# Performance work log

Hardware: AMD Instinct MI355X
Metric: run time of the kernel (lower is better)

## Reference

```python
import jax, jax.numpy as jnp
import numpy as np

B, T, U, H, M, K, C = 64, 800, 80, 512, 20, 10, 80  # batch, tsteps, char len, rnn_size, nmixtures, kmixtures, char_vec_len


def _lstm(x, W, Uw, b):
    """Keras-semantics LSTM (gate order i,f,g,o), zero initial state. x: [B,T,D] -> [B,T,H]."""
    xg = jnp.einsum('btd,dh->bth', x, W) + b  # precompute input contribution
    h0 = jnp.zeros((x.shape[0], Uw.shape[0]), x.dtype)
    c0 = jnp.zeros_like(h0)

    def step(carry, zt):
        h, c = carry
        z = zt + h @ Uw
        i, f, g, o = jnp.split(z, 4, axis=-1)
        c = jax.nn.sigmoid(f) * c + jax.nn.sigmoid(i) * jnp.tanh(g)
        h = jax.nn.sigmoid(o) * jnp.tanh(c)
        return (h, c), h

    _, hs = jax.lax.scan(step, (h0, c0), jnp.swapaxes(xg, 0, 1))
    return jnp.swapaxes(hs, 0, 1)


def _forward(stroke_data, char_seq, kappa0, W0, U0, b0, W1, U1, b1, W2, U2, b2, Wa, ba, Wm, bm):
    lstm0_out = _lstm(stroke_data, W0, U0, b0)  # [B,T,H]
    # Attention window: the per-timestep loop in the source only carries kappa,
    # which is a running sum of exp(kappa_offset) -> vectorize via cumsum.
    abk = jnp.exp(jnp.einsum('bth,hk->btk', lstm0_out, Wa) + ba)  # [B,T,3K]
    alpha, beta, koff = jnpp_split = jnp.split(abk, 3, axis=-1)
    kappa = kappa0[:, None, :, 0] + jnp.cumsum(koff, axis=1)  # [B,T,K]
    u = jnp.arange(char_seq.shape[1], dtype=stroke_data.dtype)  # [U]
    # phi: [B,T,U] = sum_k alpha * exp(-beta * (kappa - u)^2)
    phi = jnp.sum(alpha[..., None] * jnp.exp(-beta[..., None] * (kappa[..., None] - u) ** 2), axis=2)
    windows = jnp.einsum('btu,buc->btc', phi, char_seq)  # [B,T,C]
    aug = jnp.concatenate([lstm0_out, windows, stroke_data], axis=-1)
    lstm1_out = _lstm(aug, W1, U1, b1)
    lstm2_out = _lstm(lstm1_out, W2, U2, b2)
    mdn = jnp.einsum('bth,hn->btn', lstm2_out, Wm) + bm  # [B,T,1+6M]
    eos_hat = mdn[..., 0:1]
    pi_hat, mu1, mu2, s1_hat, s2_hat, rho_hat = jnp.split(mdn[..., 1:], 6, axis=-1)
    return jnp.concatenate([
        jax.nn.sigmoid(-eos_hat),
        jax.nn.softmax(pi_hat, axis=-1),
        mu1, mu2,
        jnp.exp(s1_hat), jnp.exp(s2_hat),
        jnp.tanh(rho_hat),
    ], axis=-1)  # [B,T,1+6M]


def setup_inputs() -> dict:
    key = jax.random.key(0)
    ks = jax.random.split(key, 12)
    init = lambda k, shape: jax.random.truncated_normal(k, -2.0, 2.0, shape, jnp.float32) * 0.075
    return {
        'stroke_data': jax.random.normal(ks[0], (B, T, 3), jnp.float32),
        'char_seq': jax.nn.one_hot(jax.random.randint(ks[1], (B, U), 0, C), C, dtype=jnp.float32),
        'kappa0': jnp.zeros((B, K, 1), jnp.float32),
        'W0': init(ks[2], (3, 4 * H)), 'U0': init(ks[3], (H, 4 * H)), 'b0': jnp.zeros((4 * H,)),
        'W1': init(ks[4], (H + C + 3, 4 * H)), 'U1': init(ks[5], (H, 4 * H)), 'b1': jnp.zeros((4 * H,)),
        'W2': init(ks[6], (H, 4 * H)), 'U2': init(ks[7], (H, 4 * H)), 'b2': jnp.zeros((4 * H,)),
        'Wa': init(ks[8], (H, 3 * K)),
        'ba': -3.0 + 0.25 * jax.random.truncated_normal(ks[9], -2.0, 2.0, (3 * K,), jnp.float32),
        'Wm': init(ks[10], (H, 1 + 6 * M)), 'bm': jnp.zeros((1 + 6 * M,)),
    }


def reference(stroke_data, char_seq, kappa0, W0, U0, b0, W1, U1, b1, W2, U2, b2, Wa, ba, Wm, bm):
    return _forward(stroke_data, char_seq, kappa0, W0, U0, b0, W1, U1, b1, W2, U2, b2, Wa, ba, Wm, bm)
```

## Files before the change

kernel.cpp:

```cpp
#include <hip/hip_runtime.h>

typedef unsigned short u16;
typedef unsigned int u32;
typedef short v8s __attribute__((ext_vector_type(8)));
typedef float v4f __attribute__((ext_vector_type(4)));
typedef unsigned int v4u __attribute__((ext_vector_type(4)));
typedef unsigned int v2u __attribute__((ext_vector_type(2)));

#define MFMA16 __builtin_amdgcn_mfma_f32_16x16x32_bf16

constexpr int TT = 800;
constexpr int NBLK = 178;

constexpr int AUGB  = 2240;
constexpr int AUG2B = 2048;

constexpr size_t AUGR_OFF  = 131072;
constexpr size_t AUG2R_OFF = AUGR_OFF + (size_t)4 * 64 * AUGB;
constexpr size_t WAT_OFF   = AUG2R_OFF + (size_t)4 * 64 * AUG2B;
constexpr size_t WS_ZERO   = WAT_OFF + (size_t)32 * 512 * 2;

constexpr u32 SMEM_BYTES = 82944;

enum { G_S0D = 0, G_SAD = 1, G_S1D = 2, G_S2D = 3, G_S1R = 4, G_SAR = 5, G_S2R = 6, G_SMR = 7 };

__device__ __forceinline__ float bf2f(u16 u) { return __uint_as_float(((u32)u) << 16); }
__device__ __forceinline__ u16 f2bf(float f) {
    u32 x = __float_as_uint(f);
    return (u16)((x + 0x7fffu + ((x >> 16) & 1u)) >> 16);
}
__device__ __forceinline__ short f2bfs(float f) { return (short)f2bf(f); }
__device__ __forceinline__ float sigf(float x) { return 1.f / (1.f + __expf(-x)); }
__device__ __forceinline__ float tanhf2(float x) { return 1.f - 2.f / (1.f + __expf(2.f * x)); }

__device__ __forceinline__ __amdgpu_buffer_rsrc_t mkrsrc(const void* p) {
    return __builtin_amdgcn_make_buffer_rsrc((void*)p, (short)0, -1, 0x00020000);
}
__device__ __forceinline__ v4u ldu4(__amdgpu_buffer_rsrc_t r, int off) {
    return __builtin_amdgcn_raw_buffer_load_b128(r, off, 0, 17);
}
__device__ __forceinline__ v2u ldu8(__amdgpu_buffer_rsrc_t r, int off) {
    return __builtin_amdgcn_raw_buffer_load_b64(r, off, 0, 17);
}
__device__ __forceinline__ void stq8(__amdgpu_buffer_rsrc_t r, int off, u16 a, u16 b, u16 c, u16 d) {
    v2u t; t[0] = (u32)a | ((u32)b << 16); t[1] = (u32)c | ((u32)d << 16);
    __builtin_amdgcn_raw_buffer_store_b64(t, r, off, 0, 17);
}
__device__ __forceinline__ void stq4(__amdgpu_buffer_rsrc_t r, int off, u16 a, u16 b) {
    u32 t = (u32)a | ((u32)b << 16);
    __builtin_amdgcn_raw_buffer_store_b32(t, r, off, 0, 17);
}

__device__ __forceinline__ void publish(u32* ctrl, int g, int t, int sub) {
    __hip_atomic_fetch_add(ctrl + g * 4096 + (t & 3) * 1024 + (sub & 15) * 64, 1u,
                           __ATOMIC_RELAXED, __HIP_MEMORY_SCOPE_AGENT);
}
__device__ __forceinline__ void wait4(u32* ctrl,
    int g0, int t0, u32 n0, int m0, int g1, int t1, u32 n1, int m1,
    int g2, int t2, u32 n2, int m2, int g3, int t3, u32 n3, int m3)
{
    if (threadIdx.x < 64) {
        const int lane = threadIdx.x;
        const int cl = lane >> 4, k = lane & 15;
        int g, tt, mb; u32 nn;
        if (cl == 0)      { g = g0; tt = t0; nn = n0; mb = m0; }
        else if (cl == 1) { g = g1; tt = t1; nn = n1; mb = m1; }
        else if (cl == 2) { g = g2; tt = t2; nn = n2; mb = m2; }
        else              { g = g3; tt = t3; nn = n3; mb = m3; }
        const u32 tgt = (g >= 0 && tt >= 0) ? nn * (u32)((tt >> 2) + 1) : 0u;
        u32* p = (tgt > 0) ? (ctrl + g * 4096 + (tt & 3) * 1024 + (mb + (k & 7)) * 64) : (u32*)0;
        int sp = 0;
        for (;;) {
            u32 v = p ? __hip_atomic_load(p, __ATOMIC_RELAXED, __HIP_MEMORY_SCOPE_AGENT) : 0u;
            v += __shfl_xor(v, 1); v += __shfl_xor(v, 2);
            v += __shfl_xor(v, 4); v += __shfl_xor(v, 8);
            const bool bad = (tgt > 0) && (v < tgt);
            if (__ballot(bad) == 0ull) break;
            if (sp >= 2) __builtin_amdgcn_s_sleep(4);
            else if (sp == 1) __builtin_amdgcn_s_sleep(1);
            sp++;
        }
    }
    __syncthreads();
}

__global__ void wat_init(const float* __restrict__ Wa, u16* __restrict__ WaT) {
    __amdgpu_buffer_rsrc_t r = mkrsrc(WaT);
    for (int idx = blockIdx.x * 256 + threadIdx.x; idx < 32 * 512 / 2; idx += gridDim.x * 256) {
        const int e0 = idx * 2, e1 = e0 + 1;
        const int n0 = e0 >> 9, k0 = e0 & 511;
        const int n1 = e1 >> 9, k1 = e1 & 511;
        const u16 a = (n0 < 30) ? f2bf(Wa[k0 * 30 + n0]) : (u16)0;
        const u16 b = (n1 < 30) ? f2bf(Wa[k1 * 30 + n1]) : (u16)0;
        stq4(r, idx * 4, a, b);
    }
}

__global__ __launch_bounds__(256, 1) void hw_main(
    const float* __restrict__ stroke, const float* __restrict__ charseq, const float* __restrict__ kappa0,
    const float* __restrict__ W0, const float* __restrict__ U0, const float* __restrict__ b0,
    const float* __restrict__ W1, const float* __restrict__ U1, const float* __restrict__ b1,
    const float* __restrict__ W2, const float* __restrict__ U2, const float* __restrict__ b2,
    const float* __restrict__ ba, const float* __restrict__ Wm, const float* __restrict__ bm,
    float* __restrict__ out, char* __restrict__ ws)
{
    extern __shared__ __align__(16) char smem[];
    u32* ctrl = (u32*)ws;
    u16* augr  = (u16*)(ws + AUGR_OFF);
    u16* aug2r = (u16*)(ws + AUG2R_OFF);
    const u16* WaT = (const u16*)(ws + WAT_OFF);

    const int blk = blockIdx.x, tid = threadIdx.x;
    const int wave = tid >> 6, lane = tid & 63;
    const int quad = lane >> 4, l15 = lane & 15;

    if (blk < 32) {
        const int cs = blk & 15, mg = blk >> 4;
        const int mb = mg * 8, sub = mb + (cs & 7);
        __amdgpu_buffer_rsrc_t ra = mkrsrc(augr);
        u16*   aL  = (u16*)smem;
        float* zb  = (float*)(smem + 33280);
        float* w0s = (float*)(smem + 50176);
        float* b0s = (float*)(smem + 51712);
        if (tid < 128) {
            const int cn2 = (tid >> 5) * 512 + cs * 32 + (tid & 31);
            b0s[tid] = b0[cn2];
            #pragma unroll
            for (int d = 0; d < 3; d++) w0s[d * 128 + tid] = W0[d * 2048 + cn2];
        }
        v8s bw0[16], bw1[16];
        {
            const int cnA = wave * 512 + cs * 32 + l15;
            const int cnB = cnA + 16;
            #pragma unroll
            for (int kc = 0; kc < 16; kc++)
                #pragma unroll
                for (int j = 0; j < 8; j++) {
                    const int k = kc * 32 + quad * 8 + j;
                    bw0[kc][j] = f2bfs(U0[k * 2048 + cnA]);
                    bw1[kc][j] = f2bfs(U0[k * 2048 + cnB]);
                }
        }
        float cst[4] = {0.f, 0.f, 0.f, 0.f};
        const int bl_ = tid & 31;
        const int bpre = mg * 32 + bl_;
        __syncthreads();
        #pragma unroll 1
        for (int t = 0; t < TT; t++) {
            const float xx0 = stroke[(bpre * TT + t) * 3 + 0];
            const float xx1 = stroke[(bpre * TT + t) * 3 + 1];
            const float xx2 = stroke[(bpre * TT + t) * 3 + 2];
            wait4(ctrl, G_S0D, t - 1, 32, mb, G_S1R, t - 4, 64, mb, G_SAR, t - 4, 16, mb, -1, 0, 0, 0);
            {
                const int base = (((t + 3) & 3) * 64 + mg * 32) * AUGB;
                #pragma unroll
                for (int c8 = 0; c8 < 8; c8++) {
                    const int c = tid + 256 * c8;
                    const int row = c >> 6, off = c & 63;
                    v4u d = ldu4(ra, base + row * AUGB + off * 16);
                    *(v4u*)((char*)aL + row * 1040 + off * 16) = d;
                }
            }
            __syncthreads();
            v4f c0a = {0,0,0,0}, c0b = {0,0,0,0}, c1a = {0,0,0,0}, c1b = {0,0,0,0};
            const int xo = quad * 16;
            #pragma unroll
            for (int kc = 0; kc < 16; kc++) {
                v8s x0 = *(const v8s*)((const char*)aL + l15 * 1040 + kc * 64 + xo);
                v8s x1 = *(const v8s*)((const char*)aL + (16 + l15) * 1040 + kc * 64 + xo);
                c0a = MFMA16(x0, bw0[kc], c0a, 0, 0, 0);
                c1a = MFMA16(x0, bw1[kc], c1a, 0, 0, 0);
                c0b = MFMA16(x1, bw0[kc], c0b, 0, 0, 0);
                c1b = MFMA16(x1, bw1[kc], c1b, 0, 0, 0);
            }
            const int n0 = wave * 32 + l15, n1 = n0 + 16;
            #pragma unroll
            for (int r = 0; r < 4; r++) {
                zb[(quad * 4 + r) * 132 + n0] = c0a[r];
                zb[(quad * 4 + r) * 132 + n1] = c1a[r];
                zb[(16 + quad * 4 + r) * 132 + n0] = c0b[r];
                zb[(16 + quad * 4 + r) * 132 + n1] = c1b[r];
            }
            __syncthreads();
            {
                const int bl = tid & 31, jj = tid >> 5;
                const int b = mg * 32 + bl;
                u16 hv[4];
                #pragma unroll
                for (int m = 0; m < 4; m++) {
                    const int j = jj * 4 + m;
                    float z[4];
                    #pragma unroll
                    for (int g = 0; g < 4; g++) {
                        const int n = g * 32 + j;
                        z[g] = zb[bl * 132 + n] + b0s[n] + xx0 * w0s[n] + xx1 * w0s[128 + n] + xx2 * w0s[256 + n];
                    }
                    const float cc = sigf(z[1]) * cst[m] + sigf(z[0]) * tanhf2(z[2]);
                    cst[m] = cc;
                    hv[m] = f2bf(sigf(z[3]) * tanhf2(cc));
                }
                stq8(ra, ((t & 3) * 64 + b) * AUGB + (cs * 32 + jj * 4) * 2, hv[0], hv[1], hv[2], hv[3]);
            }
            __syncthreads();
            if (tid == 0) publish(ctrl, G_S0D, t, sub);
        }
    } else if (blk < 96) {
        const int q = blk - 32, cs = q >> 1, mg = q & 1;
        const int mb = mg * 8, sub = mb + (cs & 7);
        __amdgpu_buffer_rsrc_t ra = mkrsrc(augr);
        __amdgpu_buffer_rsrc_t r2 = mkrsrc(aug2r);
        u16*   aL  = (u16*)smem;
        float* zb  = (float*)(smem + 72192);
        float* b1s = (float*)(smem + 80896);
        if (tid < 64) b1s[tid] = b1[(tid >> 4) * 512 + cs * 16 + (tid & 15)];
        v8s bw[35];
        {
            const int cn = wave * 512 + cs * 16 + l15;
            #pragma unroll
            for (int kc = 0; kc < 35; kc++)
                #pragma unroll
                for (int j = 0; j < 8; j++) {
                    const int k = kc * 32 + quad * 8 + j;
                    short v = 0;
                    if (k < 595) v = f2bfs(W1[k * 2048 + cn]);
                    else if (k >= 596 && k < 1108) v = f2bfs(U1[(k - 596) * 2048 + cn]);
                    bw[kc][j] = v;
                }
        }
        if (tid < 32) { v4u z4 = {0,0,0,0}; *(v4u*)((char*)aL + tid * 2256 + 2224) = z4; }
        float cst[2] = {0.f, 0.f};
        __syncthreads();
        #pragma unroll 1
        for (int t = 0; t < TT; t++) {
            wait4(ctrl, G_S0D, t, 32, mb, G_SAD, t, 16, mb, G_S2R, t - 4, 64, mb, -1, 0, 0, 0);
            {
                const int base = ((t & 3) * 64 + mg * 32) * AUGB;
                #pragma unroll
                for (int c10 = 0; c10 < 10; c10++) {
                    const int c = tid + 256 * c10;
                    if (c < 2400) {
                        const int row = c / 75, off = c - row * 75;
                        v4u d = ldu4(ra, base + row * AUGB + off * 16);
                        *(v4u*)((char*)aL + row * 2256 + off * 16) = d;
                    }
                }
            }
            __syncthreads();
            if (tid == 0) publish(ctrl, G_S1R, t, sub);
            wait4(ctrl, G_S1D, t - 1, 64, mb, -1, 0, 0, 0, -1, 0, 0, 0, -1, 0, 0, 0);
            {
                const int base = ((t & 3) * 64 + mg * 32) * AUGB;
                if (tid < 32) {
                    v2u d8 = ldu8(ra, base + tid * AUGB + 1192);
                    *(v2u*)((char*)aL + tid * 2256 + 1192) = d8;
                }
                #pragma unroll
                for (int c8 = 0; c8 < 8; c8++) {
                    const int c = tid + 256 * c8;
                    const int row = c >> 6, off = 75 + (c & 63);
                    v4u d = ldu4(ra, base + row * AUGB + off * 16);
                    *(v4u*)((char*)aL + row * 2256 + off * 16) = d;
                }
            }
            v4f c0 = {0,0,0,0}, c1 = {0,0,0,0};
            const int xo = quad * 16;
            #pragma unroll
            for (int kc = 0; kc < 18; kc++) {
                v8s x0 = *(const v8s*)((const char*)aL + l15 * 2256 + kc * 64 + xo);
                v8s x1 = *(const v8s*)((const char*)aL + (16 + l15) * 2256 + kc * 64 + xo);
                c0 = MFMA16(x0, bw[kc], c0, 0, 0, 0);
                c1 = MFMA16(x1, bw[kc], c1, 0, 0, 0);
            }
            __syncthreads();
            #pragma unroll
            for (int kc = 18; kc < 35; kc++) {
                v8s x0 = *(const v8s*)((const char*)aL + l15 * 2256 + kc * 64 + xo);
                v8s x1 = *(const v8s*)((const char*)aL + (16 + l15) * 2256 + kc * 64 + xo);
                c0 = MFMA16(x0, bw[kc], c0, 0, 0, 0);
                c1 = MFMA16(x1, bw[kc], c1, 0, 0, 0);
            }
            #pragma unroll
            for (int r = 0; r < 4; r++) {
                zb[(quad * 4 + r) * 68 + wave * 17 + l15] = c0[r];
                zb[(16 + quad * 4 + r) * 68 + wave * 17 + l15] = c1[r];
            }
            __syncthreads();
            {
                const int bl = tid & 31, jj = tid >> 5;
                const int b = mg * 32 + bl;
                u16 hv[2];
                #pragma unroll
                for (int m = 0; m < 2; m++) {
                    const int j = jj * 2 + m;
                    float z[4];
                    #pragma unroll
                    for (int g = 0; g < 4; g++)
                        z[g] = zb[bl * 68 + g * 17 + j] + b1s[g * 16 + j];
                    const float cc = sigf(z[1]) * cst[m] + sigf(z[0]) * tanhf2(z[2]);
                    cst[m] = cc;
                    hv[m] = f2bf(sigf(z[3]) * tanhf2(cc));
                }
                stq4(ra, (((t + 1) & 3) * 64 + b) * AUGB + (596 + cs * 16 + jj * 2) * 2, hv[0], hv[1]);
                stq4(r2, ((t & 3) * 64 + b) * AUG2B + (cs * 16 + jj * 2) * 2, hv[0], hv[1]);
            }
            __syncthreads();
            if (tid == 0) publish(ctrl, G_S1D, t, sub);
        }
    } else if (blk < 160) {
        const int q = blk - 96, cs = q >> 1, mg = q & 1;
        const int mb = mg * 8, sub = mb + (cs & 7);
        __amdgpu_buffer_rsrc_t r2 = mkrsrc(aug2r);
        u16*   aL  = (u16*)smem;
        float* zb  = (float*)(smem + 66048);
        float* b2s = (float*)(smem + 74752);
        if (tid < 64) b2s[tid] = b2[(tid >> 4) * 512 + cs * 16 + (tid & 15)];
        v8s bw[32];
        {
            const int cn = wave * 512 + cs * 16 + l15;
            #pragma unroll
            for (int kc = 0; kc < 32; kc++)
                #pragma unroll
                for (int j = 0; j < 8; j++) {
                    const int k = kc * 32 + quad * 8 + j;
                    bw[kc][j] = (k < 512) ? f2bfs(W2[k * 2048 + cn]) : f2bfs(U2[(k - 512) * 2048 + cn]);
                }
        }
        float cst[2] = {0.f, 0.f};
        __syncthreads();
        #pragma unroll 1
        for (int t = 0; t < TT; t++) {
            wait4(ctrl, G_S1D, t, 64, mb, G_SMR, t - 4, 2, mb, -1, 0, 0, 0, -1, 0, 0, 0);
            {
                const int base = ((t & 3) * 64 + mg * 32) * AUG2B;
                #pragma unroll
                for (int c8 = 0; c8 < 8; c8++) {
                    const int c = tid + 256 * c8;
                    const int row = c >> 6, off = c & 63;
                    v4u d = ldu4(r2, base + row * AUG2B + off * 16);
                    *(v4u*)((char*)aL + row * 2064 + off * 16) = d;
                }
            }
            __syncthreads();
            if (tid == 0) publish(ctrl, G_S2R, t, sub);
            wait4(ctrl, G_S2D, t - 1, 64, mb, -1, 0, 0, 0, -1, 0, 0, 0, -1, 0, 0, 0);
            {
                const int base = ((t & 3) * 64 + mg * 32) * AUG2B;
                #pragma unroll
                for (int c8 = 0; c8 < 8; c8++) {
                    const int c = tid + 256 * c8;
                    const int row = c >> 6, off = 64 + (c & 63);
                    v4u d = ldu4(r2, base + row * AUG2B + off * 16);
                    *(v4u*)((char*)aL + row * 2064 + off * 16) = d;
                }
            }
            v4f c0 = {0,0,0,0}, c1 = {0,0,0,0};
            const int xo = quad * 16;
            #pragma unroll
            for (int kc = 0; kc < 16; kc++) {
                v8s x0 = *(const v8s*)((const char*)aL + l15 * 2064 + kc * 64 + xo);
                v8s x1 = *(const v8s*)((const char*)aL + (16 + l15) * 2064 + kc * 64 + xo);
                c0 = MFMA16(x0, bw[kc], c0, 0, 0, 0);
                c1 = MFMA16(x1, bw[kc], c1, 0, 0, 0);
            }
            __syncthreads();
            #pragma unroll
            for (int kc = 16; kc < 32; kc++) {
                v8s x0 = *(const v8s*)((const char*)aL + l15 * 2064 + kc * 64 + xo);
                v8s x1 = *(const v8s*)((const char*)aL + (16 + l15) * 2064 + kc * 64 + xo);
                c0 = MFMA16(x0, bw[kc], c0, 0, 0, 0);
                c1 = MFMA16(x1, bw[kc], c1, 0, 0, 0);
            }
            #pragma unroll
            for (int r = 0; r < 4; r++) {
                zb[(quad * 4 + r) * 68 + wave * 17 + l15] = c0[r];
                zb[(16 + quad * 4 + r) * 68 + wave * 17 + l15] = c1[r];
            }
            __syncthreads();
            {
                const int bl = tid & 31, jj = tid >> 5;
                const int b = mg * 32 + bl;
                u16 hv[2];
                #pragma unroll
                for (int m = 0; m < 2; m++) {
                    const int j = jj * 2 + m;
                    float z[4];
                    #pragma unroll
                    for (int g = 0; g < 4; g++)
                        z[g] = zb[bl * 68 + g * 17 + j] + b2s[g * 16 + j];
                    const float cc = sigf(z[1]) * cst[m] + sigf(z[0]) * tanhf2(z[2]);
                    cst[m] = cc;
                    hv[m] = f2bf(sigf(z[3]) * tanhf2(cc));
                }
                stq4(r2, (((t + 1) & 3) * 64 + b) * AUG2B + (512 + cs * 16 + jj * 2) * 2, hv[0], hv[1]);
            }
            __syncthreads();
            if (tid == 0) publish(ctrl, G_S2D, t, sub);
        }
    } else if (blk < 176) {
        const int a = blk - 160;
        const int mg = a >> 3, mb = mg * 8, sub = mb + (a & 7);
        const int b = a * 4 + wave;
        __amdgpu_buffer_rsrc_t ra = mkrsrc(augr);
        u16*   watl = (u16*)smem;
        u16*   hrow = (u16*)(smem + 33280);
        float* phis = (float*)(smem + 37440);
        u16*   idxs = (u16*)(smem + 38720);
        {
            #pragma unroll
            for (int c8 = 0; c8 < 8; c8++) {
                const int c = tid + 256 * c8;
                const int row = c >> 6, off = c & 63;
                *(v4u*)((char*)watl + row * 1040 + off * 16) = *(const v4u*)(WaT + row * 512 + off * 8);
            }
        }
        #pragma unroll
        for (int rep = 0; rep < 2; rep++) {
            const int u = rep * 64 + lane;
            if (u < 80) {
                int c = 0;
                #pragma unroll 1
                for (int cc = 0; cc < 80; cc++)
                    if (charseq[b * 6400 + u * 80 + cc] > 0.5f) c = cc;
                idxs[wave * 80 + u] = (u16)c;
            }
        }
        float kap = (lane < 10) ? kappa0[b * 10 + lane] : 0.f;
        const float baf = (lane < 30) ? ba[lane] : 0.f;
        const int nn = lane & 31;
        const int k0 = (lane >> 5) * 256;
        const u16* wrow = watl + nn * 520 + k0;
        __syncthreads();
        #pragma unroll 1
        for (int t = 0; t < TT; t++) {
            float sx0 = 0.f, sx1 = 0.f;
            if (lane == 40) { sx0 = stroke[(b * TT + t) * 3 + 0]; sx1 = stroke[(b * TT + t) * 3 + 1]; }
            else if (lane == 41) { sx0 = stroke[(b * TT + t) * 3 + 2]; }
            wait4(ctrl, G_S0D, t, 32, mb, G_S1R, t - 4, 64, mb, -1, 0, 0, 0, -1, 0, 0, 0);
            {
                const int row = tid >> 6, off = tid & 63;
                v4u d = ldu4(ra, ((t & 3) * 64 + a * 4 + row) * AUGB + off * 16);
                *(v4u*)((char*)hrow + row * 1040 + off * 16) = d;
            }
            __syncthreads();
            if (tid == 0) publish(ctrl, G_SAR, t, sub);
            float acc = 0.f;
            #pragma unroll
            for (int kk = 0; kk < 32; kk++) {
                v8s hv = *(const v8s*)((const char*)hrow + wave * 1040 + (k0 + kk * 8) * 2);
                v8s wv = *(const v8s*)(wrow + kk * 8);
                #pragma unroll
                for (int e = 0; e < 8; e++) acc += bf2f((u16)hv[e]) * bf2f((u16)wv[e]);
            }
            acc += __shfl_xor(acc, 32);
            const float abk = __expf(acc + baf);
            const float kofv = __shfl(abk, 20 + (lane < 10 ? lane : 0));
            if (lane < 10) kap += kofv;
            const float u1f = (float)lane;
            float p1 = 0.f, p2 = 0.f;
            #pragma unroll
            for (int kk = 0; kk < 10; kk++) {
                const float al = __shfl(abk, kk);
                const float be = __shfl(abk, 10 + kk);
                const float kp = __shfl(kap, kk);
                const float d1 = kp - u1f, d2 = kp - (u1f + 64.f);
                p1 += al * __expf(-be * d1 * d1);
                p2 += al * __expf(-be * d2 * d2);
            }
            phis[wave * 80 + lane] = p1;
            if (lane < 16) phis[wave * 80 + 64 + lane] = p2;
            __syncthreads();
            const int db = (((t & 3) * 64 + b) * AUGB) + 512 * 2;
            if (lane < 40) {
                const int c0 = 2 * lane;
                float w0 = 0.f, w1 = 0.f;
                #pragma unroll 1
                for (int u = 0; u < 80; u++) {
                    const float pv = phis[wave * 80 + u];
                    const int ix = (int)idxs[wave * 80 + u];
                    w0 += (ix == c0)     ? pv : 0.f;
                    w1 += (ix == c0 + 1) ? pv : 0.f;
                }
                stq4(ra, db + c0 * 2, f2bf(w0), f2bf(w1));
            } else if (lane == 40) {
                stq4(ra, db + 80 * 2, f2bf(sx0), f2bf(sx1));
            } else if (lane == 41) {
                stq4(ra, db + 82 * 2, f2bf(sx0), (u16)0);
            }
            __syncthreads();
            if (tid == 0) publish(ctrl, G_SAD, t, sub);
        }
    } else {
        const int mgs = blk - 176;
        const int mb = mgs * 8, sub = mb;
        __amdgpu_buffer_rsrc_t r2 = mkrsrc(aug2r);
        u16*   aL = (u16*)smem;
        float* zb = (float*)(smem + 33280);
        v8s bw0[16], bw1[16];
        {
            const int nA = wave * 32 + l15, nB = nA + 16;
            #pragma unroll
            for (int kc = 0; kc < 16; kc++)
                #pragma unroll
                for (int j = 0; j < 8; j++) {
                    const int k = kc * 32 + quad * 8 + j;
                    bw0[kc][j] = (nA < 121) ? f2bfs(Wm[k * 121 + nA]) : (short)0;
                    bw1[kc][j] = (nB < 121) ? f2bfs(Wm[k * 121 + nB]) : (short)0;
                }
        }
        __syncthreads();
        #pragma unroll 1
        for (int t = 0; t < TT; t++) {
            wait4(ctrl, G_S2D, t, 64, mb, -1, 0, 0, 0, -1, 0, 0, 0, -1, 0, 0, 0);
            {
                const int base = (((t + 1) & 3) * 64 + mgs * 32) * AUG2B + 1024;
                #pragma unroll
                for (int c8 = 0; c8 < 8; c8++) {
                    const int c = tid + 256 * c8;
                    const int row = c >> 6, off = c & 63;
                    v4u d = ldu4(r2, base + row * AUG2B + off * 16);
                    *(v4u*)((char*)aL + row * 1040 + off * 16) = d;
                }
            }
            __syncthreads();
            if (tid == 0) publish(ctrl, G_SMR, t, sub);
            v4f c0a = {0,0,0,0}, c0b = {0,0,0,0}, c1a = {0,0,0,0}, c1b = {0,0,0,0};
            const int xo = quad * 16;
            #pragma unroll
            for (int kc = 0; kc < 16; kc++) {
                v8s x0 = *(const v8s*)((const char*)aL + l15 * 1040 + kc * 64 + xo);
                v8s x1 = *(const v8s*)((const char*)aL + (16 + l15) * 1040 + kc * 64 + xo);
                c0a = MFMA16(x0, bw0[kc], c0a, 0, 0, 0);
                c1a = MFMA16(x0, bw1[kc], c1a, 0, 0, 0);
                c0b = MFMA16(x1, bw0[kc], c0b, 0, 0, 0);
                c1b = MFMA16(x1, bw1[kc], c1b, 0, 0, 0);
            }
            const int n0 = wave * 32 + l15, n1 = n0 + 16;
            #pragma unroll
            for (int r = 0; r < 4; r++) {
                zb[(quad * 4 + r) * 132 + n0] = c0a[r];
                zb[(quad * 4 + r) * 132 + n1] = c1a[r];
                zb[(16 + quad * 4 + r) * 132 + n0] = c0b[r];
                zb[(16 + quad * 4 + r) * 132 + n1] = c1b[r];
            }
            __syncthreads();
            {
                const int b8 = tid >> 3, g8 = tid & 7;
                const int b = mgs * 32 + b8;
                const float* zr = zb + b8 * 132;
                float* orow = out + ((size_t)(b * TT + t)) * 121;
                if (g8 == 0) {
                    orow[0] = sigf(-(zr[0] + bm[0]));
                    float mx = -1e30f;
                    float zv[20];
                    #pragma unroll 1
                    for (int nl = 1; nl <= 20; nl++) { zv[nl - 1] = zr[nl] + bm[nl]; mx = fmaxf(mx, zv[nl - 1]); }
                    float ss = 0.f;
                    #pragma unroll 1
                    for (int nl = 0; nl < 20; nl++) { zv[nl] = __expf(zv[nl] - mx); ss += zv[nl]; }
                    const float inv = 1.f / ss;
                    #pragma unroll 1
                    for (int nl = 0; nl < 20; nl++) orow[nl + 1] = zv[nl] * inv;
                } else if (g8 <= 2) {
                    const int s0 = 21 + (g8 - 1) * 20;
                    #pragma unroll 1
                    for (int nl = s0; nl < s0 + 20; nl++) orow[nl] = zr[nl] + bm[nl];
                } else if (g8 <= 4) {
                    const int s0 = 61 + (g8 - 3) * 20;
                    #pragma unroll 1
                    for (int nl = s0; nl < s0 + 20; nl++) orow[nl] = __expf(zr[nl] + bm[nl]);
                } else if (g8 <= 6) {
                    const int s0 = 101 + (g8 - 5) * 10;
                    #pragma unroll 1
                    for (int nl = s0; nl < s0 + 10; nl++) orow[nl] = tanhf2(zr[nl] + bm[nl]);
                }
            }
            __syncthreads();
        }
    }
}

extern "C" void kernel_launch(void* const* d_in, const int* in_sizes, int n_in,
                              void* d_out, int out_size, void* d_ws, size_t ws_size,
                              hipStream_t stream) {
    const float* stroke  = (const float*)d_in[0];
    const float* charseq = (const float*)d_in[1];
    const float* kappa0  = (const float*)d_in[2];
    const float* W0 = (const float*)d_in[3];
    const float* U0 = (const float*)d_in[4];
    const float* b0 = (const float*)d_in[5];
    const float* W1 = (const float*)d_in[6];
    const float* U1 = (const float*)d_in[7];
    const float* b1 = (const float*)d_in[8];
    const float* W2 = (const float*)d_in[9];
    const float* U2 = (const float*)d_in[10];
    const float* b2 = (const float*)d_in[11];
    const float* Wa = (const float*)d_in[12];
    const float* ba = (const float*)d_in[13];
    const float* Wm = (const float*)d_in[14];
    const float* bm = (const float*)d_in[15];
    char* ws = (char*)d_ws;

    static bool attr_done = false;
    if (!attr_done) {
        hipFuncSetAttribute((const void*)hw_main,
                            hipFuncAttributeMaxDynamicSharedMemorySize, SMEM_BYTES);
        attr_done = true;
    }

    hipMemsetAsync(d_ws, 0, WS_ZERO, stream);
    wat_init<<<8, 256, 0, stream>>>(Wa, (u16*)(ws + WAT_OFF));
    hw_main<<<NBLK, 256, SMEM_BYTES, stream>>>(stroke, charseq, kappa0, W0, U0, b0,
                                               W1, U1, b1, W2, U2, b2, ba, Wm, bm,
                                               (float*)d_out, ws);
}
```

Baseline: 8.748 ms.

## Split shared activation buffers into per-producer-block tiled layouts and use uncached polling

Replaces the row-major augmented activation buffers with separate per-layer buffers (h0, window, h1, h2), each laid out by producer column slice so every producer block writes one contiguous chunk and consumers gather tiles into LDS. The layer-1 K layout is realigned so the window/stroke segment is padded to a 32-wide chunk boundary. The window block now zero-fills the padding. Flag polling switches to an inline-asm buffer load with sc0/sc1 cache-bypass bits and a shorter sleep, aiming to cut cross-block sync latency and scattered small global writes. Risks include more complex gather indexing and more polling traffic.

```diff
diff --git a/kernel.cpp b/kernel.cpp
--- a/kernel.cpp
+++ b/kernel.cpp
@@ -12,15 +12,14 @@
 constexpr int TT = 800;
 constexpr int NBLK = 178;
 
-constexpr int AUGB  = 2240;
-constexpr int AUG2B = 2048;
-
-constexpr size_t AUGR_OFF  = 131072;
-constexpr size_t AUG2R_OFF = AUGR_OFF + (size_t)4 * 64 * AUGB;
-constexpr size_t WAT_OFF   = AUG2R_OFF + (size_t)4 * 64 * AUG2B;
-constexpr size_t WS_ZERO   = WAT_OFF + (size_t)32 * 512 * 2;
-
-constexpr u32 SMEM_BYTES = 82944;
+constexpr size_t H0_OFF  = 131072;
+constexpr size_t WIN_OFF = H0_OFF  + (size_t)4 * 2 * 16 * 2048;
+constexpr size_t H1_OFF  = WIN_OFF + (size_t)4 * 2 * 32 * 256;
+constexpr size_t H2_OFF  = H1_OFF  + (size_t)4 * 2 * 32 * 1024;
+constexpr size_t WAT_OFF = H2_OFF  + (size_t)4 * 2 * 32 * 1024;
+constexpr size_t WS_ZERO = WAT_OFF + (size_t)32 * 512 * 2;
+
+constexpr u32 SMEM_BYTES = 81920;
 
 enum { G_S0D = 0, G_SAD = 1, G_S1D = 2, G_S2D = 3, G_S1R = 4, G_SAR = 5, G_S2R = 6, G_SMR = 7 };
 
@@ -39,9 +38,6 @@
 __device__ __forceinline__ v4u ldu4(__amdgpu_buffer_rsrc_t r, int off) {
     return __builtin_amdgcn_raw_buffer_load_b128(r, off, 0, 17);
 }
-__device__ __forceinline__ v2u ldu8(__amdgpu_buffer_rsrc_t r, int off) {
-    return __builtin_amdgcn_raw_buffer_load_b64(r, off, 0, 17);
-}
 __device__ __forceinline__ void stq8(__amdgpu_buffer_rsrc_t r, int off, u16 a, u16 b, u16 c, u16 d) {
     v2u t; t[0] = (u32)a | ((u32)b << 16); t[1] = (u32)c | ((u32)d << 16);
     __builtin_amdgcn_raw_buffer_store_b64(t, r, off, 0, 17);
@@ -49,6 +45,22 @@
 __device__ __forceinline__ void stq4(__amdgpu_buffer_rsrc_t r, int off, u16 a, u16 b) {
     u32 t = (u32)a | ((u32)b << 16);
     __builtin_amdgcn_raw_buffer_store_b32(t, r, off, 0, 17);
+}
+
+__device__ __forceinline__ v4u mksrd(const void* p) {
+    v4u r;
+    r[0] = (u32)(size_t)p;
+    r[1] = (u32)((size_t)p >> 32);
+    r[2] = 0xFFFFFFFFu;
+    r[3] = 0x00020000u;
+    return r;
+}
+__device__ __forceinline__ u32 poll_ld(v4u srd, int off) {
+    u32 v;
+    asm volatile("buffer_load_dword %0, %1, %2, 0 offen sc0 sc1\n\t"
+                 "s_waitcnt vmcnt(0)"
+                 : "=v"(v) : "v"(off), "s"(srd) : "memory");
+    return v;
 }
 
 __device__ __forceinline__ void publish(u32* ctrl, int g, int t, int sub) {
@@ -68,15 +80,16 @@
         else if (cl == 2) { g = g2; tt = t2; nn = n2; mb = m2; }
         else              { g = g3; tt = t3; nn = n3; mb = m3; }
         const u32 tgt = (g >= 0 && tt >= 0) ? nn * (u32)((tt >> 2) + 1) : 0u;
-        u32* p = (tgt > 0) ? (ctrl + g * 4096 + (tt & 3) * 1024 + (mb + (k & 7)) * 64) : (u32*)0;
+        const v4u srd = mksrd(ctrl);
+        const int boff = (g >= 0) ? (g * 4096 + ((tt & 3)) * 1024 + (mb + (k & 7)) * 64) * 4 : 0;
         int sp = 0;
         for (;;) {
-            u32 v = p ? __hip_atomic_load(p, __ATOMIC_RELAXED, __HIP_MEMORY_SCOPE_AGENT) : 0u;
+            u32 v = (tgt > 0) ? poll_ld(srd, boff) : 0u;
             v += __shfl_xor(v, 1); v += __shfl_xor(v, 2);
             v += __shfl_xor(v, 4); v += __shfl_xor(v, 8);
             const bool bad = (tgt > 0) && (v < tgt);
             if (__ballot(bad) == 0ull) break;
-            if (sp >= 2) __builtin_amdgcn_s_sleep(4);
+            if (sp >= 2) __builtin_amdgcn_s_sleep(2);
             else if (sp == 1) __builtin_amdgcn_s_sleep(1);
             sp++;
         }
@@ -106,8 +119,10 @@
 {
     extern __shared__ __align__(16) char smem[];
     u32* ctrl = (u32*)ws;
-    u16* augr  = (u16*)(ws + AUGR_OFF);
-    u16* aug2r = (u16*)(ws + AUG2R_OFF);
+    u16* h0b  = (u16*)(ws + H0_OFF);
+    u16* winb = (u16*)(ws + WIN_OFF);
+    u16* h1b  = (u16*)(ws + H1_OFF);
+    u16* h2b  = (u16*)(ws + H2_OFF);
     const u16* WaT = (const u16*)(ws + WAT_OFF);
 
     const int blk = blockIdx.x, tid = threadIdx.x;
@@ -117,7 +132,7 @@
     if (blk < 32) {
         const int cs = blk & 15, mg = blk >> 4;
         const int mb = mg * 8, sub = mb + (cs & 7);
-        __amdgpu_buffer_rsrc_t ra = mkrsrc(augr);
+        __amdgpu_buffer_rsrc_t rh0 = mkrsrc(h0b);
         u16*   aL  = (u16*)smem;
         float* zb  = (float*)(smem + 33280);
         float* w0s = (float*)(smem + 50176);
@@ -142,8 +157,7 @@
                 }
         }
         float cst[4] = {0.f, 0.f, 0.f, 0.f};
-        const int bl_ = tid & 31;
-        const int bpre = mg * 32 + bl_;
+        const int bpre = mg * 32 + (tid & 31);
         __syncthreads();
         #pragma unroll 1
         for (int t = 0; t < TT; t++) {
@@ -152,13 +166,14 @@
             const float xx2 = stroke[(bpre * TT + t) * 3 + 2];
             wait4(ctrl, G_S0D, t - 1, 32, mb, G_S1R, t - 4, 64, mb, G_SAR, t - 4, 16, mb, -1, 0, 0, 0);
             {
-                const int base = (((t + 3) & 3) * 64 + mg * 32) * AUGB;
+                const int base = ((((t + 3) & 3) * 2 + mg) * 16) * 2048;
                 #pragma unroll
                 for (int c8 = 0; c8 < 8; c8++) {
                     const int c = tid + 256 * c8;
-                    const int row = c >> 6, off = c & 63;
-                    v4u d = ldu4(ra, base + row * AUGB + off * 16);
-                    *(v4u*)((char*)aL + row * 1040 + off * 16) = d;
+                    const int cs_ = c >> 7, w = c & 127;
+                    const int row = w >> 2, col16 = w & 3;
+                    v4u d = ldu4(rh0, base + cs_ * 2048 + w * 16);
+                    *(v4u*)((char*)aL + row * 1040 + cs_ * 64 + col16 * 16) = d;
                 }
             }
             __syncthreads();
@@ -184,7 +199,6 @@
             __syncthreads();
             {
                 const int bl = tid & 31, jj = tid >> 5;
-                const int b = mg * 32 + bl;
                 u16 hv[4];
                 #pragma unroll
                 for (int m = 0; m < 4; m++) {
@@ -199,7 +213,8 @@
                     cst[m] = cc;
                     hv[m] = f2bf(sigf(z[3]) * tanhf2(cc));
                 }
-                stq8(ra, ((t & 3) * 64 + b) * AUGB + (cs * 32 + jj * 4) * 2, hv[0], hv[1], hv[2], hv[3]);
+                const int off = (((t & 3) * 2 + mg) * 16 + cs) * 2048 + bl * 64 + jj * 8;
+                stq8(rh0, off, hv[0], hv[1], hv[2], hv[3]);
             }
             __syncthreads();
             if (tid == 0) publish(ctrl, G_S0D, t, sub);
@@ -207,8 +222,9 @@
     } else if (blk < 96) {
         const int q = blk - 32, cs = q >> 1, mg = q & 1;
         const int mb = mg * 8, sub = mb + (cs & 7);
-        __amdgpu_buffer_rsrc_t ra = mkrsrc(augr);
-        __amdgpu_buffer_rsrc_t r2 = mkrsrc(aug2r);
+        __amdgpu_buffer_rsrc_t rh0 = mkrsrc(h0b);
+        __amdgpu_buffer_rsrc_t rw  = mkrsrc(winb);
+        __amdgpu_buffer_rsrc_t rh1 = mkrsrc(h1b);
         u16*   aL  = (u16*)smem;
         float* zb  = (float*)(smem + 72192);
         float* b1s = (float*)(smem + 80896);
@@ -222,26 +238,34 @@
                 for (int j = 0; j < 8; j++) {
                     const int k = kc * 32 + quad * 8 + j;
                     short v = 0;
-                    if (k < 595) v = f2bfs(W1[k * 2048 + cn]);
-                    else if (k >= 596 && k < 1108) v = f2bfs(U1[(k - 596) * 2048 + cn]);
+                    if (kc < 19) { if (k < 595) v = f2bfs(W1[k * 2048 + cn]); }
+                    else v = f2bfs(U1[(k - 608) * 2048 + cn]);
                     bw[kc][j] = v;
                 }
         }
-        if (tid < 32) { v4u z4 = {0,0,0,0}; *(v4u*)((char*)aL + tid * 2256 + 2224) = z4; }
         float cst[2] = {0.f, 0.f};
         __syncthreads();
         #pragma unroll 1
         for (int t = 0; t < TT; t++) {
             wait4(ctrl, G_S0D, t, 32, mb, G_SAD, t, 16, mb, G_S2R, t - 4, 64, mb, -1, 0, 0, 0);
             {
-                const int base = ((t & 3) * 64 + mg * 32) * AUGB;
-                #pragma unroll
-                for (int c10 = 0; c10 < 10; c10++) {
-                    const int c = tid + 256 * c10;
-                    if (c < 2400) {
-                        const int row = c / 75, off = c - row * 75;
-                        v4u d = ldu4(ra, base + row * AUGB + off * 16);
-                        *(v4u*)((char*)aL + row * 2256 + off * 16) = d;
+                const int baseH = (((t & 3) * 2 + mg) * 16) * 2048;
+                const int baseW = (((t & 3) * 2 + mg) * 32) * 256;
+                #pragma unroll
+                for (int c8 = 0; c8 < 8; c8++) {
+                    const int c = tid + 256 * c8;
+                    const int cs_ = c >> 7, w = c & 127;
+                    const int row = w >> 2, col16 = w & 3;
+                    v4u d = ldu4(rh0, baseH + cs_ * 2048 + w * 16);
+                    *(v4u*)((char*)aL + row * 2256 + cs_ * 64 + col16 * 16) = d;
+                }
+                #pragma unroll
+                for (int c2 = 0; c2 < 2; c2++) {
+                    const int c = tid + 256 * c2;
+                    if (c < 384) {
+                        const int row = c / 12, off = c - row * 12;
+                        v4u d = ldu4(rw, baseW + row * 256 + off * 16);
+                        *(v4u*)((char*)aL + row * 2256 + 1024 + off * 16) = d;
                     }
                 }
             }
@@ -249,23 +273,20 @@
             if (tid == 0) publish(ctrl, G_S1R, t, sub);
             wait4(ctrl, G_S1D, t - 1, 64, mb, -1, 0, 0, 0, -1, 0, 0, 0, -1, 0, 0, 0);
             {
-                const int base = ((t & 3) * 64 + mg * 32) * AUGB;
-                if (tid < 32) {
-                    v2u d8 = ldu8(ra, base + tid * AUGB + 1192);
-                    *(v2u*)((char*)aL + tid * 2256 + 1192) = d8;
-                }
+                const int baseP = ((((t + 3) & 3) * 2 + mg) * 32) * 1024;
                 #pragma unroll
                 for (int c8 = 0; c8 < 8; c8++) {
                     const int c = tid + 256 * c8;
-                    const int row = c >> 6, off = 75 + (c & 63);
-                    v4u d = ldu4(ra, base + row * AUGB + off * 16);
-                    *(v4u*)((char*)aL + row * 2256 + off * 16) = d;
+                    const int cs_ = c >> 6, w = c & 63;
+                    const int row = w >> 1, col16 = w & 1;
+                    v4u d = ldu4(rh1, baseP + cs_ * 1024 + w * 16);
+                    *(v4u*)((char*)aL + row * 2256 + 1216 + cs_ * 32 + col16 * 16) = d;
                 }
             }
             v4f c0 = {0,0,0,0}, c1 = {0,0,0,0};
             const int xo = quad * 16;
             #pragma unroll
-            for (int kc = 0; kc < 18; kc++) {
+            for (int kc = 0; kc < 19; kc++) {
                 v8s x0 = *(const v8s*)((const char*)aL + l15 * 2256 + kc * 64 + xo);
                 v8s x1 = *(const v8s*)((const char*)aL + (16 + l15) * 2256 + kc * 64 + xo);
                 c0 = MFMA16(x0, bw[kc], c0, 0, 0, 0);
@@ -273,7 +294,7 @@
             }
             __syncthreads();
             #pragma unroll
-            for (int kc = 18; kc < 35; kc++) {
+            for (int kc = 19; kc < 35; kc++) {
                 v8s x0 = *(const v8s*)((const char*)aL + l15 * 2256 + kc * 64 + xo);
                 v8s x1 = *(const v8s*)((const char*)aL + (16 + l15) * 2256 + kc * 64 + xo);
                 c0 = MFMA16(x0, bw[kc], c0, 0, 0, 0);
@@ -287,7 +308,6 @@
             __syncthreads();
             {
                 const int bl = tid & 31, jj = tid >> 5;
-                const int b = mg * 32 + bl;
                 u16 hv[2];
                 #pragma unroll
                 for (int m = 0; m < 2; m++) {
@@ -300,8 +320,8 @@
                     cst[m] = cc;
                     hv[m] = f2bf(sigf(z[3]) * tanhf2(cc));
                 }
-                stq4(ra, (((t + 1) & 3) * 64 + b) * AUGB + (596 + cs * 16 + jj * 2) * 2, hv[0], hv[1]);
-                stq4(r2, ((t & 3) * 64 + b) * AUG2B + (cs * 16 + jj * 2) * 2, hv[0], hv[1]);
+                const int off = (((t & 3) * 2 + mg) * 32 + cs) * 1024 + bl * 32 + jj * 4;
+                stq4(rh1, off, hv[0], hv[1]);
             }
             __syncthreads();
             if (tid == 0) publish(ctrl, G_S1D, t, sub);
@@ -309,7 +329,8 @@
     } else if (blk < 160) {
         const int q = blk - 96, cs = q >> 1, mg = q & 1;
         const int mb = mg * 8, sub = mb + (cs & 7);
-        __amdgpu_buffer_rsrc_t r2 = mkrsrc(aug2r);
+        __amdgpu_buffer_rsrc_t rh1 = mkrsrc(h1b);
+        __amdgpu_buffer_rsrc_t rh2 = mkrsrc(h2b);
         u16*   aL  = (u16*)smem;
         float* zb  = (float*)(smem + 66048);
         float* b2s = (float*)(smem + 74752);
@@ -331,26 +352,28 @@
         for (int t = 0; t < TT; t++) {
             wait4(ctrl, G_S1D, t, 64, mb, G_SMR, t - 4, 2, mb, -1, 0, 0, 0, -1, 0, 0, 0);
             {
-                const int base = ((t & 3) * 64 + mg * 32) * AUG2B;
+                const int baseP = (((t & 3) * 2 + mg) * 32) * 1024;
                 #pragma unroll
                 for (int c8 = 0; c8 < 8; c8++) {
                     const int c = tid + 256 * c8;
-                    const int row = c >> 6, off = c & 63;
-                    v4u d = ldu4(r2, base + row * AUG2B + off * 16);
-                    *(v4u*)((char*)aL + row * 2064 + off * 16) = d;
+                    const int cs_ = c >> 6, w = c & 63;
+                    const int row = w >> 1, col16 = w & 1;
+                    v4u d = ldu4(rh1, baseP + cs_ * 1024 + w * 16);
+                    *(v4u*)((char*)aL + row * 2064 + cs_ * 32 + col16 * 16) = d;
                 }
             }
             __syncthreads();
             if (tid == 0) publish(ctrl, G_S2R, t, sub);
             wait4(ctrl, G_S2D, t - 1, 64, mb, -1, 0, 0, 0, -1, 0, 0, 0, -1, 0, 0, 0);
             {
-                const int base = ((t & 3) * 64 + mg * 32) * AUG2B;
+                const int baseP = ((((t + 3) & 3) * 2 + mg) * 32) * 1024;
                 #pragma unroll
                 for (int c8 = 0; c8 < 8; c8++) {
                     const int c = tid + 256 * c8;
-                    const int row = c >> 6, off = 64 + (c & 63);
-                    v4u d = ldu4(r2, base + row * AUG2B + off * 16);
-                    *(v4u*)((char*)aL + row * 2064 + off * 16) = d;
+                    const int cs_ = c >> 6, w = c & 63;
+                    const int row = w >> 1, col16 = w & 1;
+                    v4u d = ldu4(rh2, baseP + cs_ * 1024 + w * 16);
+                    *(v4u*)((char*)aL + row * 2064 + 1024 + cs_ * 32 + col16 * 16) = d;
                 }
             }
             v4f c0 = {0,0,0,0}, c1 = {0,0,0,0};
@@ -378,7 +401,6 @@
             __syncthreads();
             {
                 const int bl = tid & 31, jj = tid >> 5;
-                const int b = mg * 32 + bl;
                 u16 hv[2];
                 #pragma unroll
                 for (int m = 0; m < 2; m++) {
@@ -391,7 +413,8 @@
                     cst[m] = cc;
                     hv[m] = f2bf(sigf(z[3]) * tanhf2(cc));
                 }
-                stq4(r2, (((t + 1) & 3) * 64 + b) * AUG2B + (512 + cs * 16 + jj * 2) * 2, hv[0], hv[1]);
+                const int off = (((t & 3) * 2 + mg) * 32 + cs) * 1024 + bl * 32 + jj * 4;
+                stq4(rh2, off, hv[0], hv[1]);
             }
             __syncthreads();
             if (tid == 0) publish(ctrl, G_S2D, t, sub);
@@ -400,7 +423,9 @@
         const int a = blk - 160;
         const int mg = a >> 3, mb = mg * 8, sub = mb + (a & 7);
         const int b = a * 4 + wave;
-        __amdgpu_buffer_rsrc_t ra = mkrsrc(augr);
+        const int rloc = (a & 7) * 4 + wave;
+        __amdgpu_buffer_rsrc_t rh0 = mkrsrc(h0b);
+        __amdgpu_buffer_rsrc_t rw  = mkrsrc(winb);
         u16*   watl = (u16*)smem;
         u16*   hrow = (u16*)(smem + 33280);
         float* phis = (float*)(smem + 37440);
@@ -437,9 +462,12 @@
             else if (lane == 41) { sx0 = stroke[(b * TT + t) * 3 + 2]; }
             wait4(ctrl, G_S0D, t, 32, mb, G_S1R, t - 4, 64, mb, -1, 0, 0, 0, -1, 0, 0, 0);
             {
-                const int row = tid >> 6, off = tid & 63;
-                v4u d = ldu4(ra, ((t & 3) * 64 + a * 4 + row) * AUGB + off * 16);
-                *(v4u*)((char*)hrow + row * 1040 + off * 16) = d;
+                const int base = (((t & 3) * 2 + mg) * 16) * 2048;
+                const int row = tid >> 6, q6 = tid & 63;
+                const int cs_ = q6 >> 2, col16 = q6 & 3;
+                const int rl = (a & 7) * 4 + row;
+                v4u d = ldu4(rh0, base + cs_ * 2048 + rl * 64 + col16 * 16);
+                *(v4u*)((char*)hrow + row * 1040 + cs_ * 64 + col16 * 16) = d;
             }
             __syncthreads();
             if (tid == 0) publish(ctrl, G_SAR, t, sub);
@@ -469,7 +497,7 @@
             phis[wave * 80 + lane] = p1;
             if (lane < 16) phis[wave * 80 + 64 + lane] = p2;
             __syncthreads();
-            const int db = (((t & 3) * 64 + b) * AUGB) + 512 * 2;
+            const int db = (((t & 3) * 2 + mg) * 32 + rloc) * 256;
             if (lane < 40) {
                 const int c0 = 2 * lane;
                 float w0 = 0.f, w1 = 0.f;
@@ -480,11 +508,13 @@
                     w0 += (ix == c0)     ? pv : 0.f;
                     w1 += (ix == c0 + 1) ? pv : 0.f;
                 }
-                stq4(ra, db + c0 * 2, f2bf(w0), f2bf(w1));
+                stq4(rw, db + c0 * 2, f2bf(w0), f2bf(w1));
             } else if (lane == 40) {
-                stq4(ra, db + 80 * 2, f2bf(sx0), f2bf(sx1));
+                stq4(rw, db + 160, f2bf(sx0), f2bf(sx1));
             } else if (lane == 41) {
-                stq4(ra, db + 82 * 2, f2bf(sx0), (u16)0);
+                stq4(rw, db + 164, f2bf(sx0), (u16)0);
+            } else if (lane < 48) {
+                stq4(rw, db + 168 + (lane - 42) * 4, (u16)0, (u16)0);
             }
             __syncthreads();
             if (tid == 0) publish(ctrl, G_SAD, t, sub);
@@ -492,7 +522,7 @@
     } else {
         const int mgs = blk - 176;
         const int mb = mgs * 8, sub = mb;
-        __amdgpu_buffer_rsrc_t r2 = mkrsrc(aug2r);
+        __amdgpu_buffer_rsrc_t rh2 = mkrsrc(h2b);
         u16*   aL = (u16*)smem;
         float* zb = (float*)(smem + 33280);
         v8s bw0[16], bw1[16];
@@ -512,13 +542,14 @@
         for (int t = 0; t < TT; t++) {
             wait4(ctrl, G_S2D, t, 64, mb, -1, 0, 0, 0, -1, 0, 0, 0, -1, 0, 0, 0);
             {
-                const int base = (((t + 1) & 3) * 64 + mgs * 32) * AUG2B + 1024;
+                const int baseP = (((t & 3) * 2 + mgs) * 32) * 1024;
                 #pragma unroll
                 for (int c8 = 0; c8 < 8; c8++) {
                     const int c = tid + 256 * c8;
-                    const int row = c >> 6, off = c & 63;
-                    v4u d = ldu4(r2, base + row * AUG2B + off * 16);
-                    *(v4u*)((char*)aL + row * 1040 + off * 16) = d;
+                    const int cs_ = c >> 6, w = c & 63;
+                    const int row = w >> 1, col16 = w & 1;
+                    v4u d = ldu4(rh2, baseP + cs_ * 1024 + w * 16);
+                    *(v4u*)((char*)aL + row * 1040 + cs_ * 32 + col16 * 16) = d;
                 }
             }
             __syncthreads();
```

After: 8.622 ms. Within noise of the previous version (-1.4%).
